# Optimization experiments

Measured on AMD Instinct MI355X. Metric: run time of the kernel, lower is better.

## Reference

```python
import jax, jax.numpy as jnp
import numpy as np

VOCAB, EMB, UNITS = 2000, 64, 512
B, T = 64, 128

def lstm(x_emb, Wx, Wh, b, h0, c0):
    """Keras LSTM: gates order (i, f, g, o), sigmoid recurrent activation, tanh activation.
    x_emb: [B, T, EMB]. Returns (H [B,T,U], h [B,U], c [B,U])."""
    # Precompute input contribution for all timesteps (one big GEMM)
    xz = jnp.einsum('bte,eu->btu', x_emb, Wx) + b  # [B, T, 4U]

    def step(carry, xz_t):
        h, c = carry
        z = xz_t + h @ Wh  # [B, 4U]
        i, f, g, o = jnp.split(z, 4, axis=-1)
        i = jax.nn.sigmoid(i)
        f = jax.nn.sigmoid(f)
        g = jnp.tanh(g)
        o = jax.nn.sigmoid(o)
        c = f * c + i * g
        h = o * jnp.tanh(c)
        return (h, c), h

    (h, c), H = jax.lax.scan(step, (h0, c0), jnp.swapaxes(xz, 0, 1))
    return jnp.swapaxes(H, 0, 1), h, c


def setup_inputs() -> dict:
    key = jax.random.key(0)
    ks = jax.random.split(key, 10)
    s = 0.05
    return {
        'x': jax.random.randint(ks[0], (B, T), 0, VOCAB),
        'y': jax.random.randint(ks[1], (B, T), 0, VOCAB),
        'enc_emb': jax.random.normal(ks[2], (VOCAB, EMB), jnp.float32) * s,
        'enc_Wx': jax.random.normal(ks[3], (EMB, 4 * UNITS), jnp.float32) * s,
        'enc_Wh': jax.random.normal(ks[4], (UNITS, 4 * UNITS), jnp.float32) * s,
        'enc_b': jnp.zeros((4 * UNITS,), jnp.float32),
        'dec_emb': jax.random.normal(ks[5], (VOCAB, EMB), jnp.float32) * s,
        'dec_Wx': jax.random.normal(ks[6], (EMB, 4 * UNITS), jnp.float32) * s,
        'dec_Wh': jax.random.normal(ks[7], (UNITS, 4 * UNITS), jnp.float32) * s,
        'dec_b': jnp.zeros((4 * UNITS,), jnp.float32),
        'dense_W': jax.random.normal(ks[8], (2 * UNITS, VOCAB), jnp.float32) * s,
        'dense_b': jnp.zeros((VOCAB,), jnp.float32),
    }


def reference(x, y, enc_emb, enc_Wx, enc_Wh, enc_b,
              dec_emb, dec_Wx, dec_Wh, dec_b, dense_W, dense_b):
    z0 = jnp.zeros((x.shape[0], UNITS), jnp.float32)
    # Encoder
    H, h, c = lstm(enc_emb[x], enc_Wx, enc_Wh, enc_b, z0, z0)  # H: [B,T,U]
    # Decoder LSTM
    s0 = h
    S, h2, c2 = lstm(dec_emb[y], dec_Wx, dec_Wh, dec_b, h, c)  # S: [B,T,U]
    # Shifted states as attention queries (teacher forcing, Luong dot-attention)
    S_ = jnp.concatenate([s0[:, None, :], S[:, :-1, :]], axis=1)  # [B,T,U]
    scores = jnp.einsum('bqu,bku->bqk', S_, H)  # [B,T,T]
    A = jnp.einsum('bqk,bku->bqu', jax.nn.softmax(scores, axis=-1), H)
    yo = jnp.concatenate([S, A], axis=-1)  # [B,T,2U]
    return jax.nn.softmax(yo @ dense_W + dense_b, axis=-1)  # [B,T,VOCAB]
```

## Files before the change

kernel.cpp:

```cpp
#include <hip/hip_runtime.h>
#include <math.h>

#define NB 64
#define NT 128
#define NE 64
#define NU 512
#define NG 2048
#define NV 2000
#define BU (NB*NU)
#define GRID_LSTM 256
#define KTOT 576
#define HS 584
#define WSTRIDE 584
#define SMEM_BYTES (64*WSTRIDE*2 + 16*HS*2 + 2*8*64*4)

typedef __attribute__((ext_vector_type(8))) short bf16x8;
typedef __attribute__((ext_vector_type(4))) float f32x4;
typedef __attribute__((ext_vector_type(8))) unsigned short u16x8;

__device__ __forceinline__ unsigned short f2bf(float x) {
    unsigned int u = __float_as_uint(x);
    u += 0x7FFFu + ((u >> 16) & 1u);
    return (unsigned short)(u >> 16);
}
__device__ __forceinline__ float fsigmoid(float x) {
    return __builtin_amdgcn_rcpf(1.f + __expf(-x));
}
__device__ __forceinline__ float ftanh(float x) {
    return 1.f - 2.f * __builtin_amdgcn_rcpf(__expf(2.f * x) + 1.f);
}

__global__ __launch_bounds__(512, 1)
void lstm_coop(const int* __restrict__ ids, const unsigned short* __restrict__ embb,
               const unsigned short* __restrict__ WhT,
               const float* __restrict__ bias,
               const float* __restrict__ h0, const float* __restrict__ c0,
               float* __restrict__ Hout, float* __restrict__ hping,
               float* __restrict__ cfin, unsigned int* __restrict__ flags)
{
    extern __shared__ char smem[];
    unsigned short* whb  = (unsigned short*)smem;
    unsigned short* hlds = (unsigned short*)(smem + 64 * WSTRIDE * 2);
    float* zbuf = (float*)(smem + 64 * WSTRIDE * 2 + 16 * HS * 2);

    const int tid  = threadIdx.x;
    const int wv   = tid >> 6;
    const int cl   = tid & 63;
    const int bk   = blockIdx.x;
    const int rg   = bk & 7;
    const int cgi  = bk >> 3;
    const int brow0 = rg * 8;
    const int u0    = cgi * 16;

    const int bl  = tid >> 4;
    const int uug = tid & 15;
    float creg = 0.f;
    float b4[4] = {0.f, 0.f, 0.f, 0.f};
    if (tid < 128) {
#pragma unroll
        for (int g = 0; g < 4; ++g) b4[g] = bias[g * 512 + u0 + uug];
        if (c0) creg = c0[(brow0 + bl) * NU + u0 + uug];
    }

    {
        const int cp = tid >> 3, ch = tid & 7;
        const int cg = (cp >> 4) * 512 + u0 + (cp & 15);
        const uint4* src = reinterpret_cast<const uint4*>(WhT + (size_t)cg * KTOT + ch * 72);
        uint4* dst = reinterpret_cast<uint4*>(whb + cp * WSTRIDE + ch * 72);
#pragma unroll
        for (int i = 0; i < 9; ++i) dst[i] = src[i];
    }

    const int col = wv * 64 + cl;
#pragma unroll
    for (int b = 0; b < 8; ++b)
        hlds[b * HS + col] = h0 ? f2bf(h0[(brow0 + b) * NU + col]) : (unsigned short)0;
    for (int i = tid; i < 8 * HS; i += 512) hlds[8 * HS + i] = 0;
    {
        const int idb = ids[(brow0 + wv) * NT + 0];
        hlds[wv * HS + 512 + cl] = embb[(size_t)idb * NE + cl];
    }
    unsigned int* fl = flags + rg * 64;

    for (int t = 0; t < NT; ++t) {
        __syncthreads();

        {
            const int g = wv & 3, half = wv >> 2;
            const int rr = cl & 15, kh = cl >> 4;
            f32x4 acc = {0.f, 0.f, 0.f, 0.f};
            const unsigned short* arow = hlds + rr * HS;
            const unsigned short* brow = whb + (g * 16 + rr) * WSTRIDE;
#pragma unroll
            for (int kt = 0; kt < 9; ++kt) {
                const int kb = (half * 9 + kt) * 32 + kh * 8;
                bf16x8 af = *reinterpret_cast<const bf16x8*>(arow + kb);
                bf16x8 bf = *reinterpret_cast<const bf16x8*>(brow + kb);
                acc = __builtin_amdgcn_mfma_f32_16x16x32_bf16(af, bf, acc, 0, 0, 0);
            }
            if (cl < 32) {
#pragma unroll
                for (int reg = 0; reg < 4; ++reg)
                    zbuf[half * 512 + (kh * 4 + reg) * 64 + g * 16 + rr] = acc[reg];
            }
        }
        __syncthreads();

        float h_ = 0.f;
        if (tid < 128) {
            float z[4];
#pragma unroll
            for (int g = 0; g < 4; ++g)
                z[g] = b4[g] + zbuf[bl * 64 + g * 16 + uug]
                             + zbuf[512 + bl * 64 + g * 16 + uug];
            const float i_ = fsigmoid(z[0]);
            const float f_ = fsigmoid(z[1]);
            const float g_ = ftanh(z[2]);
            const float o_ = fsigmoid(z[3]);
            creg = f_ * creg + i_ * g_;
            h_ = o_ * ftanh(creg);
            float* hw = hping + ((t + 1) & 1) * BU;
            __hip_atomic_store(&hw[(brow0 + bl) * NU + u0 + uug], h_,
                               __ATOMIC_RELAXED, __HIP_MEMORY_SCOPE_AGENT);
        }
        if (t == NT - 1) {
            if (tid < 128)
                Hout[((size_t)(brow0 + bl) * NT + t) * NU + u0 + uug] = h_;
            break;
        }

        if (tid < 128)
            asm volatile("s_waitcnt vmcnt(0)" ::: "memory");
        __syncthreads();

        if (tid < 128 && (tid & 63) == 0)
            __hip_atomic_store(&fl[(tid >> 6) * 32 + cgi], (unsigned)(t + 1),
                               __ATOMIC_RELAXED, __HIP_MEMORY_SCOPE_AGENT);
        if (tid < 128)
            Hout[((size_t)(brow0 + bl) * NT + t) * NU + u0 + uug] = h_;

        {
            const int idb = ids[(brow0 + wv) * NT + (t + 1)];
            hlds[wv * HS + 512 + cl] = embb[(size_t)idb * NE + cl];
        }

        if (wv == 0) {
            const unsigned target = (unsigned)(t + 1);
            while (true) {
                unsigned v = __hip_atomic_load(&fl[cl], __ATOMIC_RELAXED,
                                               __HIP_MEMORY_SCOPE_AGENT);
#pragma unroll
                for (int o = 16; o; o >>= 1) {
                    unsigned v2 = (unsigned)__shfl_xor((int)v, o);
                    v = v2 < v ? v2 : v;
                }
                if (v >= target) break;
                __builtin_amdgcn_s_sleep(1);
            }
        }
        __syncthreads();

        {
            const float* hr = hping + ((t + 1) & 1) * BU + (size_t)brow0 * NU;
            float tmp[8];
#pragma unroll
            for (int b = 0; b < 8; ++b)
                tmp[b] = __hip_atomic_load(const_cast<float*>(&hr[b * NU + col]),
                                           __ATOMIC_RELAXED, __HIP_MEMORY_SCOPE_AGENT);
#pragma unroll
            for (int b = 0; b < 8; ++b) hlds[b * HS + col] = f2bf(tmp[b]);
        }
    }
    if (tid < 128) cfin[(brow0 + bl) * NU + u0 + uug] = creg;
}

__global__ __launch_bounds__(256)
void conv_emb(const float* __restrict__ e, unsigned short* __restrict__ o, int n)
{
    const int i = (blockIdx.x * 256 + threadIdx.x) * 8;
    if (i >= n) return;
    const float4 v0 = reinterpret_cast<const float4*>(e + i)[0];
    const float4 v1 = reinterpret_cast<const float4*>(e + i)[1];
    u16x8 r;
    r[0] = f2bf(v0.x); r[1] = f2bf(v0.y); r[2] = f2bf(v0.z); r[3] = f2bf(v0.w);
    r[4] = f2bf(v1.x); r[5] = f2bf(v1.y); r[6] = f2bf(v1.z); r[7] = f2bf(v1.w);
    *reinterpret_cast<u16x8*>(o + i) = r;
}

__global__ __launch_bounds__(256)
void conv_WhT(const float* __restrict__ Wh, const float* __restrict__ Wx,
              unsigned short* __restrict__ WhT)
{
    __shared__ float lt[64][65];
    const int tid = threadIdx.x;
    const int c0 = blockIdx.x * 64;
    const int k0 = blockIdx.y * 64;
#pragma unroll
    for (int j = 0; j < 16; ++j) {
        const int lin = tid + 256 * j;
        const int kk = lin >> 6, cc = lin & 63;
        const int k = k0 + kk;
        lt[cc][kk] = (k < 512) ? Wh[(size_t)k * NG + c0 + cc]
                               : Wx[(size_t)(k - 512) * NG + c0 + cc];
    }
    __syncthreads();
    const int c = tid >> 2, kseg = tid & 3;
    unsigned short tmp[16];
#pragma unroll
    for (int m = 0; m < 16; ++m)
        tmp[m] = f2bf(lt[c][kseg * 16 + m]);
    unsigned short* dst = WhT + (size_t)(c0 + c) * KTOT + k0 + kseg * 16;
    *reinterpret_cast<u16x8*>(dst)     = *reinterpret_cast<u16x8*>(tmp);
    *reinterpret_cast<u16x8*>(dst + 8) = *reinterpret_cast<u16x8*>(tmp + 8);
}

__global__ __launch_bounds__(256)
void attn_kernel(const float* __restrict__ S, const float* __restrict__ Hbuf,
                 const float* __restrict__ s0, float* __restrict__ A)
{
    const int tid  = threadIdx.x;
    const int wv   = tid >> 6;
    const int lane = tid & 63;
    const int b    = blockIdx.x >> 5;
    const int q    = (blockIdx.x & 31) * 4 + wv;

    const float* qrow = (q == 0) ? (s0 + (size_t)b * NU)
                                 : (S + ((size_t)b * NT + (q - 1)) * NU);
    const float4* q4 = reinterpret_cast<const float4*>(qrow);
    const float4 qa = q4[lane], qb = q4[64 + lane];
    const float4* Hb = reinterpret_cast<const float4*>(Hbuf + (size_t)b * NT * NU);

    float sr0 = 0.f, sr1 = 0.f;
    for (int k = 0; k < NT; ++k) {
        const float4* hk = Hb + (size_t)k * 128;
        float4 ha = hk[lane], hc = hk[64 + lane];
        float d = qa.x * ha.x + qa.y * ha.y + qa.z * ha.z + qa.w * ha.w
                + qb.x * hc.x + qb.y * hc.y + qb.z * hc.z + qb.w * hc.w;
#pragma unroll
        for (int o = 32; o; o >>= 1) d += __shfl_xor(d, o);
        if ((k & 63) == lane) { if (k < 64) sr0 = d; else sr1 = d; }
        if ((k & 31) == 31) __syncthreads();
    }

    float m = fmaxf(sr0, sr1);
#pragma unroll
    for (int o = 32; o; o >>= 1) m = fmaxf(m, __shfl_xor(m, o));
    float e0 = expf(sr0 - m), e1 = expf(sr1 - m);
    float s = e0 + e1;
#pragma unroll
    for (int o = 32; o; o >>= 1) s += __shfl_xor(s, o);
    const float inv = 1.f / s;
    e0 *= inv; e1 *= inv;

    float4 acc0 = {0.f, 0.f, 0.f, 0.f}, acc1 = {0.f, 0.f, 0.f, 0.f};
    for (int k = 0; k < 64; ++k) {
        const float wk = __shfl(e0, k);
        const float4* hk = Hb + (size_t)k * 128;
        float4 ha = hk[lane], hc = hk[64 + lane];
        acc0.x += wk * ha.x; acc0.y += wk * ha.y; acc0.z += wk * ha.z; acc0.w += wk * ha.w;
        acc1.x += wk * hc.x; acc1.y += wk * hc.y; acc1.z += wk * hc.z; acc1.w += wk * hc.w;
        if ((k & 31) == 31) __syncthreads();
    }
    for (int k = 0; k < 64; ++k) {
        const float wk = __shfl(e1, k);
        const float4* hk = Hb + (size_t)(64 + k) * 128;
        float4 ha = hk[lane], hc = hk[64 + lane];
        acc0.x += wk * ha.x; acc0.y += wk * ha.y; acc0.z += wk * ha.z; acc0.w += wk * ha.w;
        acc1.x += wk * hc.x; acc1.y += wk * hc.y; acc1.z += wk * hc.z; acc1.w += wk * hc.w;
        if ((k & 31) == 31) __syncthreads();
    }
    float4* Aq = reinterpret_cast<float4*>(A + ((size_t)b * NT + q) * NU);
    Aq[lane] = acc0;
    Aq[64 + lane] = acc1;
}

__global__ __launch_bounds__(256)
void conv_yo(const float* __restrict__ S, const float* __restrict__ A,
             unsigned short* __restrict__ yo)
{
    const int base = (blockIdx.x * 256 + threadIdx.x) * 8;
    const int row = base >> 10;
    const int col = base & 1023;
    const float* src = (col < 512) ? (S + (size_t)row * NU + col)
                                   : (A + (size_t)row * NU + (col - 512));
    const float4 v0 = reinterpret_cast<const float4*>(src)[0];
    const float4 v1 = reinterpret_cast<const float4*>(src)[1];
    u16x8 o;
    o[0] = f2bf(v0.x); o[1] = f2bf(v0.y); o[2] = f2bf(v0.z); o[3] = f2bf(v0.w);
    o[4] = f2bf(v1.x); o[5] = f2bf(v1.y); o[6] = f2bf(v1.z); o[7] = f2bf(v1.w);
    *reinterpret_cast<u16x8*>(yo + base) = o;
}

__global__ __launch_bounds__(256)
void conv_Wt(const float* __restrict__ W, unsigned short* __restrict__ Wt)
{
    __shared__ float lt[64][65];
    const int tid = threadIdx.x;
    const int c0 = blockIdx.x * 64;
    const int k0 = blockIdx.y * 64;
#pragma unroll
    for (int j = 0; j < 16; ++j) {
        const int lin = tid + 256 * j;
        const int kk = lin >> 6, cc = lin & 63;
        const int c = c0 + cc;
        lt[cc][kk] = (c < NV) ? W[(size_t)(k0 + kk) * NV + c] : 0.f;
    }
    __syncthreads();
    const int c = tid >> 2, kseg = tid & 3;
    unsigned short tmp[16];
#pragma unroll
    for (int m = 0; m < 16; ++m)
        tmp[m] = f2bf(lt[c][kseg * 16 + m]);
    unsigned short* dst = Wt + (size_t)(c0 + c) * 1024 + k0 + kseg * 16;
    *reinterpret_cast<u16x8*>(dst)     = *reinterpret_cast<u16x8*>(tmp);
    *reinterpret_cast<u16x8*>(dst + 8) = *reinterpret_cast<u16x8*>(tmp + 8);
}

__global__ __launch_bounds__(256)
void dense_mfma(const unsigned short* __restrict__ yo,
                const unsigned short* __restrict__ Wt,
                const float* __restrict__ bias, float* __restrict__ out)
{
    __shared__ unsigned short Asm[128][40];
    __shared__ unsigned short Bsm[128][40];
    const int tid  = threadIdx.x;
    const int wave = tid >> 6, lane = tid & 63;
    const int wm = wave >> 1, wn = wave & 1;
    const int r0 = blockIdx.y * 128, c0 = blockIdx.x * 128;
    const int rr = lane & 15, kh = lane >> 4;

    f32x4 acc[4][4];
#pragma unroll
    for (int m = 0; m < 4; ++m)
#pragma unroll
        for (int n = 0; n < 4; ++n) acc[m][n] = (f32x4){0.f, 0.f, 0.f, 0.f};

    for (int k0 = 0; k0 < 1024; k0 += 32) {
        __syncthreads();
#pragma unroll
        for (int h = 0; h < 2; ++h) {
            const int row = (tid >> 2) + h * 64, seg = tid & 3;
            *reinterpret_cast<uint4*>(&Asm[row][seg * 8]) =
                *reinterpret_cast<const uint4*>(yo + (size_t)(r0 + row) * 1024 + k0 + seg * 8);
            *reinterpret_cast<uint4*>(&Bsm[row][seg * 8]) =
                *reinterpret_cast<const uint4*>(Wt + (size_t)(c0 + row) * 1024 + k0 + seg * 8);
        }
        __syncthreads();
        bf16x8 af[4], bfr[4];
#pragma unroll
        for (int m = 0; m < 4; ++m)
            af[m] = *reinterpret_cast<const bf16x8*>(&Asm[wm * 64 + m * 16 + rr][kh * 8]);
#pragma unroll
        for (int n = 0; n < 4; ++n)
            bfr[n] = *reinterpret_cast<const bf16x8*>(&Bsm[wn * 64 + n * 16 + rr][kh * 8]);
#pragma unroll
        for (int m = 0; m < 4; ++m)
#pragma unroll
            for (int n = 0; n < 4; ++n)
                acc[m][n] = __builtin_amdgcn_mfma_f32_16x16x32_bf16(af[m], bfr[n], acc[m][n], 0, 0, 0);
    }

#pragma unroll
    for (int m = 0; m < 4; ++m) {
#pragma unroll
        for (int n = 0; n < 4; ++n) {
            const int c = c0 + wn * 64 + n * 16 + rr;
            if (c < NV) {
                const float bc = bias[c];
#pragma unroll
                for (int reg = 0; reg < 4; ++reg) {
                    const int r = r0 + wm * 64 + m * 16 + kh * 4 + reg;
                    out[(size_t)r * NV + c] = acc[m][n][reg] + bc;
                }
            }
        }
    }
}

__global__ __launch_bounds__(256)
void softmax_rows(float* __restrict__ out)
{
    __shared__ float red[4];
    const int t = threadIdx.x;
    float* row = out + (size_t)blockIdx.x * NV;

    float v[8];
    float m = -INFINITY;
#pragma unroll
    for (int i = 0; i < 8; ++i) {
        const int j = t + 256 * i;
        v[i] = (j < NV) ? row[j] : -INFINITY;
        m = fmaxf(m, v[i]);
    }
#pragma unroll
    for (int o = 32; o; o >>= 1) m = fmaxf(m, __shfl_xor(m, o));
    if ((t & 63) == 0) red[t >> 6] = m;
    __syncthreads();
    m = fmaxf(fmaxf(red[0], red[1]), fmaxf(red[2], red[3]));
    __syncthreads();

    float s = 0.f;
#pragma unroll
    for (int i = 0; i < 8; ++i) {
        const int j = t + 256 * i;
        if (j < NV) { v[i] = expf(v[i] - m); s += v[i]; }
    }
#pragma unroll
    for (int o = 32; o; o >>= 1) s += __shfl_xor(s, o);
    if ((t & 63) == 0) red[t >> 6] = s;
    __syncthreads();
    const float inv = 1.f / (red[0] + red[1] + red[2] + red[3]);
#pragma unroll
    for (int i = 0; i < 8; ++i) {
        const int j = t + 256 * i;
        if (j < NV) row[j] = v[i] * inv;
    }
}

extern "C" void kernel_launch(void* const* d_in, const int* in_sizes, int n_in,
                              void* d_out, int out_size, void* d_ws, size_t ws_size,
                              hipStream_t stream)
{
    const int*   x       = (const int*)  d_in[0];
    const int*   y       = (const int*)  d_in[1];
    const float* enc_emb = (const float*)d_in[2];
    const float* enc_Wx  = (const float*)d_in[3];
    const float* enc_Wh  = (const float*)d_in[4];
    const float* enc_b   = (const float*)d_in[5];
    const float* dec_emb = (const float*)d_in[6];
    const float* dec_Wx  = (const float*)d_in[7];
    const float* dec_Wh  = (const float*)d_in[8];
    const float* dec_b   = (const float*)d_in[9];
    const float* dns_W   = (const float*)d_in[10];
    const float* dns_b   = (const float*)d_in[11];
    float* out = (float*)d_out;

    float* ws   = (float*)d_ws;
    float* Hbuf = ws;
    float* Sbuf = Hbuf + (size_t)NB * NT * NU;
    float* Abuf = Sbuf + (size_t)NB * NT * NU;
    unsigned short* Wt = (unsigned short*)(Abuf + (size_t)NB * NT * NU);
    float* ehp  = (float*)(Wt + (size_t)2048 * 1024);
    float* dhp  = ehp + 2 * BU;
    float* cfe  = dhp + 2 * BU;
    float* cfd  = cfe + BU;
    unsigned int* bar0 = (unsigned int*)(cfd + BU);
    unsigned int* bar1 = bar0 + 512;
    unsigned short* WhT_e = (unsigned short*)(bar1 + 512);
    unsigned short* WhT_d = WhT_e + (size_t)2048 * KTOT;
    unsigned short* embb_e = WhT_d + (size_t)2048 * KTOT;
    unsigned short* embb_d = embb_e + (size_t)NV * NE;
    unsigned short* yo = (unsigned short*)Hbuf;

    hipMemsetAsync(bar0, 0, 2 * 512 * sizeof(unsigned int), stream);

    (void)hipFuncSetAttribute(reinterpret_cast<const void*>(lstm_coop),
                              hipFuncAttributeMaxDynamicSharedMemorySize, SMEM_BYTES);

    conv_emb<<<dim3((NV * NE / 8 + 255) / 256), dim3(256), 0, stream>>>(enc_emb, embb_e, NV * NE);
    conv_emb<<<dim3((NV * NE / 8 + 255) / 256), dim3(256), 0, stream>>>(dec_emb, embb_d, NV * NE);
    conv_WhT<<<dim3(32, 9), dim3(256), 0, stream>>>(enc_Wh, enc_Wx, WhT_e);
    conv_WhT<<<dim3(32, 9), dim3(256), 0, stream>>>(dec_Wh, dec_Wx, WhT_d);
    conv_Wt<<<dim3(32, 16), dim3(256), 0, stream>>>(dns_W, Wt);

    const float* nul = nullptr;
    {
        void* args[] = { (void*)&x, (void*)&embb_e, (void*)&WhT_e, (void*)&enc_b,
                         (void*)&nul, (void*)&nul,
                         (void*)&Hbuf, (void*)&ehp, (void*)&cfe, (void*)&bar0 };
        (void)hipLaunchCooperativeKernel(reinterpret_cast<void*>(lstm_coop),
                                         dim3(GRID_LSTM), dim3(512), args,
                                         SMEM_BYTES, stream);
    }
    {
        const float* h0 = ehp;
        const float* c0 = cfe;
        void* args[] = { (void*)&y, (void*)&embb_d, (void*)&WhT_d, (void*)&dec_b,
                         (void*)&h0, (void*)&c0,
                         (void*)&Sbuf, (void*)&dhp, (void*)&cfd, (void*)&bar1 };
        (void)hipLaunchCooperativeKernel(reinterpret_cast<void*>(lstm_coop),
                                         dim3(GRID_LSTM), dim3(512), args,
                                         SMEM_BYTES, stream);
    }
    attn_kernel<<<dim3(NB * 32), dim3(256), 0, stream>>>(Sbuf, Hbuf, ehp, Abuf);
    conv_yo<<<dim3(4096), dim3(256), 0, stream>>>(Sbuf, Abuf, yo);
    dense_mfma<<<dim3(16, 64), dim3(256), 0, stream>>>(yo, Wt, dns_b, out);
    softmax_rows<<<dim3(NB * NT), dim3(256), 0, stream>>>(out);
}
```

Measured before the change: 998.5 us.

## Fuse encoder and decoder LSTMs into one cooperative kernel and merge conversions

Runs the encoder and decoder recurrences in a single persistent cooperative kernel over 2*T steps. At the boundary it reloads the decoder weights and bias into shared memory while keeping the cell state and h in registers and LDS. This removes one cooperative launch and the global round-trip of the final h and c. It also merges the paired embedding and weight conversion kernels into single launches, and folds the fp32-to-bf16 conversion of [S,A] into the dense GEMM's tile load, dropping the conv_yo pass. The risk is that the dense loader now reads fp32 with per-element conversion, which means more global traffic per tile.

```diff
diff --git a/kernel.cpp b/kernel.cpp
--- a/kernel.cpp
+++ b/kernel.cpp
@@ -31,12 +31,15 @@
 }
 
 __global__ __launch_bounds__(512, 1)
-void lstm_coop(const int* __restrict__ ids, const unsigned short* __restrict__ embb,
-               const unsigned short* __restrict__ WhT,
-               const float* __restrict__ bias,
-               const float* __restrict__ h0, const float* __restrict__ c0,
-               float* __restrict__ Hout, float* __restrict__ hping,
-               float* __restrict__ cfin, unsigned int* __restrict__ flags)
+void lstm2_coop(const int* __restrict__ xids, const int* __restrict__ yids,
+                const unsigned short* __restrict__ embb_e,
+                const unsigned short* __restrict__ embb_d,
+                const unsigned short* __restrict__ WhT_e,
+                const unsigned short* __restrict__ WhT_d,
+                const float* __restrict__ enc_b, const float* __restrict__ dec_b,
+                float* __restrict__ Hbuf, float* __restrict__ Sbuf,
+                float* __restrict__ hping, float* __restrict__ hfin,
+                unsigned int* __restrict__ flags)
 {
     extern __shared__ char smem[];
     unsigned short* whb  = (unsigned short*)smem;
@@ -58,14 +61,13 @@
     float b4[4] = {0.f, 0.f, 0.f, 0.f};
     if (tid < 128) {
 #pragma unroll
-        for (int g = 0; g < 4; ++g) b4[g] = bias[g * 512 + u0 + uug];
-        if (c0) creg = c0[(brow0 + bl) * NU + u0 + uug];
+        for (int g = 0; g < 4; ++g) b4[g] = enc_b[g * 512 + u0 + uug];
     }
 
     {
         const int cp = tid >> 3, ch = tid & 7;
         const int cg = (cp >> 4) * 512 + u0 + (cp & 15);
-        const uint4* src = reinterpret_cast<const uint4*>(WhT + (size_t)cg * KTOT + ch * 72);
+        const uint4* src = reinterpret_cast<const uint4*>(WhT_e + (size_t)cg * KTOT + ch * 72);
         uint4* dst = reinterpret_cast<uint4*>(whb + cp * WSTRIDE + ch * 72);
 #pragma unroll
         for (int i = 0; i < 9; ++i) dst[i] = src[i];
@@ -73,16 +75,17 @@
 
     const int col = wv * 64 + cl;
 #pragma unroll
-    for (int b = 0; b < 8; ++b)
-        hlds[b * HS + col] = h0 ? f2bf(h0[(brow0 + b) * NU + col]) : (unsigned short)0;
+    for (int b = 0; b < 8; ++b) hlds[b * HS + col] = 0;
     for (int i = tid; i < 8 * HS; i += 512) hlds[8 * HS + i] = 0;
     {
-        const int idb = ids[(brow0 + wv) * NT + 0];
-        hlds[wv * HS + 512 + cl] = embb[(size_t)idb * NE + cl];
+        const int idb = xids[(brow0 + wv) * NT + 0];
+        hlds[wv * HS + 512 + cl] = embb_e[(size_t)idb * NE + cl];
     }
     unsigned int* fl = flags + rg * 64;
 
-    for (int t = 0; t < NT; ++t) {
+    for (int T = 0; T < 2 * NT; ++T) {
+        const int t = T & (NT - 1);
+        float* Ho = (T < NT) ? Hbuf : Sbuf;
         __syncthreads();
 
         {
@@ -119,13 +122,13 @@
             const float o_ = fsigmoid(z[3]);
             creg = f_ * creg + i_ * g_;
             h_ = o_ * ftanh(creg);
-            float* hw = hping + ((t + 1) & 1) * BU;
+            float* hw = hping + ((T + 1) & 1) * BU;
             __hip_atomic_store(&hw[(brow0 + bl) * NU + u0 + uug], h_,
                                __ATOMIC_RELAXED, __HIP_MEMORY_SCOPE_AGENT);
         }
-        if (t == NT - 1) {
+        if (T == 2 * NT - 1) {
             if (tid < 128)
-                Hout[((size_t)(brow0 + bl) * NT + t) * NU + u0 + uug] = h_;
+                Ho[((size_t)(brow0 + bl) * NT + t) * NU + u0 + uug] = h_;
             break;
         }
 
@@ -134,18 +137,24 @@
         __syncthreads();
 
         if (tid < 128 && (tid & 63) == 0)
-            __hip_atomic_store(&fl[(tid >> 6) * 32 + cgi], (unsigned)(t + 1),
+            __hip_atomic_store(&fl[(tid >> 6) * 32 + cgi], (unsigned)(T + 1),
                                __ATOMIC_RELAXED, __HIP_MEMORY_SCOPE_AGENT);
-        if (tid < 128)
-            Hout[((size_t)(brow0 + bl) * NT + t) * NU + u0 + uug] = h_;
+        if (tid < 128) {
+            Ho[((size_t)(brow0 + bl) * NT + t) * NU + u0 + uug] = h_;
+            if (T == NT - 1)
+                hfin[(brow0 + bl) * NU + u0 + uug] = h_;
+        }
 
         {
-            const int idb = ids[(brow0 + wv) * NT + (t + 1)];
-            hlds[wv * HS + 512 + cl] = embb[(size_t)idb * NE + cl];
+            const int Tn = T + 1;
+            const int* nids = (Tn < NT) ? xids : yids;
+            const unsigned short* nemb = (Tn < NT) ? embb_e : embb_d;
+            const int idb = nids[(brow0 + wv) * NT + (Tn & (NT - 1))];
+            hlds[wv * HS + 512 + cl] = nemb[(size_t)idb * NE + cl];
         }
 
         if (wv == 0) {
-            const unsigned target = (unsigned)(t + 1);
+            const unsigned target = (unsigned)(T + 1);
             while (true) {
                 unsigned v = __hip_atomic_load(&fl[cl], __ATOMIC_RELAXED,
                                                __HIP_MEMORY_SCOPE_AGENT);
@@ -161,7 +170,7 @@
         __syncthreads();
 
         {
-            const float* hr = hping + ((t + 1) & 1) * BU + (size_t)brow0 * NU;
+            const float* hr = hping + ((T + 1) & 1) * BU + (size_t)brow0 * NU;
             float tmp[8];
 #pragma unroll
             for (int b = 0; b < 8; ++b)
@@ -170,14 +179,31 @@
 #pragma unroll
             for (int b = 0; b < 8; ++b) hlds[b * HS + col] = f2bf(tmp[b]);
         }
-    }
-    if (tid < 128) cfin[(brow0 + bl) * NU + u0 + uug] = creg;
-}
-
-__global__ __launch_bounds__(256)
-void conv_emb(const float* __restrict__ e, unsigned short* __restrict__ o, int n)
-{
-    const int i = (blockIdx.x * 256 + threadIdx.x) * 8;
+
+        if (T == NT - 1) {
+            const int cp = tid >> 3, ch = tid & 7;
+            const int cg = (cp >> 4) * 512 + u0 + (cp & 15);
+            const uint4* src = reinterpret_cast<const uint4*>(WhT_d + (size_t)cg * KTOT + ch * 72);
+            uint4* dst = reinterpret_cast<uint4*>(whb + cp * WSTRIDE + ch * 72);
+#pragma unroll
+            for (int i = 0; i < 9; ++i) dst[i] = src[i];
+            if (tid < 128) {
+#pragma unroll
+                for (int g = 0; g < 4; ++g) b4[g] = dec_b[g * 512 + u0 + uug];
+            }
+        }
+    }
+}
+
+__global__ __launch_bounds__(256)
+void conv_emb2(const float* __restrict__ e0, const float* __restrict__ e1,
+               unsigned short* __restrict__ o0, unsigned short* __restrict__ o1,
+               int n, int nbh)
+{
+    int b = blockIdx.x;
+    const float* e = e0; unsigned short* o = o0;
+    if (b >= nbh) { b -= nbh; e = e1; o = o1; }
+    const int i = (b * 256 + threadIdx.x) * 8;
     if (i >= n) return;
     const float4 v0 = reinterpret_cast<const float4*>(e + i)[0];
     const float4 v1 = reinterpret_cast<const float4*>(e + i)[1];
@@ -188,10 +214,14 @@
 }
 
 __global__ __launch_bounds__(256)
-void conv_WhT(const float* __restrict__ Wh, const float* __restrict__ Wx,
-              unsigned short* __restrict__ WhT)
+void conv_WhT2(const float* __restrict__ Wh_e, const float* __restrict__ Wx_e,
+               const float* __restrict__ Wh_d, const float* __restrict__ Wx_d,
+               unsigned short* __restrict__ WhT_e, unsigned short* __restrict__ WhT_d)
 {
     __shared__ float lt[64][65];
+    const float* Wh = (blockIdx.z == 0) ? Wh_e : Wh_d;
+    const float* Wx = (blockIdx.z == 0) ? Wx_e : Wx_d;
+    unsigned short* WhT = (blockIdx.z == 0) ? WhT_e : WhT_d;
     const int tid = threadIdx.x;
     const int c0 = blockIdx.x * 64;
     const int k0 = blockIdx.y * 64;
@@ -275,23 +305,6 @@
 }
 
 __global__ __launch_bounds__(256)
-void conv_yo(const float* __restrict__ S, const float* __restrict__ A,
-             unsigned short* __restrict__ yo)
-{
-    const int base = (blockIdx.x * 256 + threadIdx.x) * 8;
-    const int row = base >> 10;
-    const int col = base & 1023;
-    const float* src = (col < 512) ? (S + (size_t)row * NU + col)
-                                   : (A + (size_t)row * NU + (col - 512));
-    const float4 v0 = reinterpret_cast<const float4*>(src)[0];
-    const float4 v1 = reinterpret_cast<const float4*>(src)[1];
-    u16x8 o;
-    o[0] = f2bf(v0.x); o[1] = f2bf(v0.y); o[2] = f2bf(v0.z); o[3] = f2bf(v0.w);
-    o[4] = f2bf(v1.x); o[5] = f2bf(v1.y); o[6] = f2bf(v1.z); o[7] = f2bf(v1.w);
-    *reinterpret_cast<u16x8*>(yo + base) = o;
-}
-
-__global__ __launch_bounds__(256)
 void conv_Wt(const float* __restrict__ W, unsigned short* __restrict__ Wt)
 {
     __shared__ float lt[64][65];
@@ -317,7 +330,7 @@
 }
 
 __global__ __launch_bounds__(256)
-void dense_mfma(const unsigned short* __restrict__ yo,
+void dense_mfma(const float* __restrict__ S, const float* __restrict__ A,
                 const unsigned short* __restrict__ Wt,
                 const float* __restrict__ bias, float* __restrict__ out)
 {
@@ -340,8 +353,15 @@
 #pragma unroll
         for (int h = 0; h < 2; ++h) {
             const int row = (tid >> 2) + h * 64, seg = tid & 3;
-            *reinterpret_cast<uint4*>(&Asm[row][seg * 8]) =
-                *reinterpret_cast<const uint4*>(yo + (size_t)(r0 + row) * 1024 + k0 + seg * 8);
+            const int kc = k0 + seg * 8;
+            const float* asrc = (kc < 512) ? (S + (size_t)(r0 + row) * NU + kc)
+                                           : (A + (size_t)(r0 + row) * NU + (kc - 512));
+            const float4 a0 = reinterpret_cast<const float4*>(asrc)[0];
+            const float4 a1 = reinterpret_cast<const float4*>(asrc)[1];
+            u16x8 av;
+            av[0] = f2bf(a0.x); av[1] = f2bf(a0.y); av[2] = f2bf(a0.z); av[3] = f2bf(a0.w);
+            av[4] = f2bf(a1.x); av[5] = f2bf(a1.y); av[6] = f2bf(a1.z); av[7] = f2bf(a1.w);
+            *reinterpret_cast<u16x8*>(&Asm[row][seg * 8]) = av;
             *reinterpret_cast<uint4*>(&Bsm[row][seg * 8]) =
                 *reinterpret_cast<const uint4*>(Wt + (size_t)(c0 + row) * 1024 + k0 + seg * 8);
         }
@@ -440,50 +460,34 @@
     float* Sbuf = Hbuf + (size_t)NB * NT * NU;
     float* Abuf = Sbuf + (size_t)NB * NT * NU;
     unsigned short* Wt = (unsigned short*)(Abuf + (size_t)NB * NT * NU);
-    float* ehp  = (float*)(Wt + (size_t)2048 * 1024);
-    float* dhp  = ehp + 2 * BU;
-    float* cfe  = dhp + 2 * BU;
-    float* cfd  = cfe + BU;
-    unsigned int* bar0 = (unsigned int*)(cfd + BU);
-    unsigned int* bar1 = bar0 + 512;
-    unsigned short* WhT_e = (unsigned short*)(bar1 + 512);
+    float* hping = (float*)(Wt + (size_t)2048 * 1024);
+    float* hfin  = hping + 2 * BU;
+    unsigned int* bar0 = (unsigned int*)(hfin + BU);
+    unsigned short* WhT_e = (unsigned short*)(bar0 + 512);
     unsigned short* WhT_d = WhT_e + (size_t)2048 * KTOT;
     unsigned short* embb_e = WhT_d + (size_t)2048 * KTOT;
     unsigned short* embb_d = embb_e + (size_t)NV * NE;
-    unsigned short* yo = (unsigned short*)Hbuf;
-
-    hipMemsetAsync(bar0, 0, 2 * 512 * sizeof(unsigned int), stream);
-
-    (void)hipFuncSetAttribute(reinterpret_cast<const void*>(lstm_coop),
+
+    hipMemsetAsync(bar0, 0, 512 * sizeof(unsigned int), stream);
+
+    (void)hipFuncSetAttribute(reinterpret_cast<const void*>(lstm2_coop),
                               hipFuncAttributeMaxDynamicSharedMemorySize, SMEM_BYTES);
 
-    conv_emb<<<dim3((NV * NE / 8 + 255) / 256), dim3(256), 0, stream>>>(enc_emb, embb_e, NV * NE);
-    conv_emb<<<dim3((NV * NE / 8 + 255) / 256), dim3(256), 0, stream>>>(dec_emb, embb_d, NV * NE);
-    conv_WhT<<<dim3(32, 9), dim3(256), 0, stream>>>(enc_Wh, enc_Wx, WhT_e);
-    conv_WhT<<<dim3(32, 9), dim3(256), 0, stream>>>(dec_Wh, dec_Wx, WhT_d);
+    const int nemb = NV * NE, nbh = (nemb / 8 + 255) / 256;
+    conv_emb2<<<dim3(2 * nbh), dim3(256), 0, stream>>>(enc_emb, dec_emb, embb_e, embb_d, nemb, nbh);
+    conv_WhT2<<<dim3(32, 9, 2), dim3(256), 0, stream>>>(enc_Wh, enc_Wx, dec_Wh, dec_Wx, WhT_e, WhT_d);
     conv_Wt<<<dim3(32, 16), dim3(256), 0, stream>>>(dns_W, Wt);
 
-    const float* nul = nullptr;
     {
-        void* args[] = { (void*)&x, (void*)&embb_e, (void*)&WhT_e, (void*)&enc_b,
-                         (void*)&nul, (void*)&nul,
-                         (void*)&Hbuf, (void*)&ehp, (void*)&cfe, (void*)&bar0 };
-        (void)hipLaunchCooperativeKernel(reinterpret_cast<void*>(lstm_coop),
+        void* args[] = { (void*)&x, (void*)&y, (void*)&embb_e, (void*)&embb_d,
+                         (void*)&WhT_e, (void*)&WhT_d, (void*)&enc_b, (void*)&dec_b,
+                         (void*)&Hbuf, (void*)&Sbuf, (void*)&hping, (void*)&hfin,
+                         (void*)&bar0 };
+        (void)hipLaunchCooperativeKernel(reinterpret_cast<void*>(lstm2_coop),
                                          dim3(GRID_LSTM), dim3(512), args,
                                          SMEM_BYTES, stream);
     }
-    {
-        const float* h0 = ehp;
-        const float* c0 = cfe;
-        void* args[] = { (void*)&y, (void*)&embb_d, (void*)&WhT_d, (void*)&dec_b,
-                         (void*)&h0, (void*)&c0,
-                         (void*)&Sbuf, (void*)&dhp, (void*)&cfd, (void*)&bar1 };
-        (void)hipLaunchCooperativeKernel(reinterpret_cast<void*>(lstm_coop),
-                                         dim3(GRID_LSTM), dim3(512), args,
-                                         SMEM_BYTES, stream);
-    }
-    attn_kernel<<<dim3(NB * 32), dim3(256), 0, stream>>>(Sbuf, Hbuf, ehp, Abuf);
-    conv_yo<<<dim3(4096), dim3(256), 0, stream>>>(Sbuf, Abuf, yo);
-    dense_mfma<<<dim3(16, 64), dim3(256), 0, stream>>>(yo, Wt, dns_b, out);
+    attn_kernel<<<dim3(NB * 32), dim3(256), 0, stream>>>(Sbuf, Hbuf, hfin, Abuf);
+    dense_mfma<<<dim3(16, 64), dim3(256), 0, stream>>>(Sbuf, Abuf, Wt, dns_b, out);
     softmax_rows<<<dim3(NB * NT), dim3(256), 0, stream>>>(out);
 }
```

New measurement: 985.0 us. Within noise of the previous version (-1.3%).
